# Kernel tuning notes

Measured on AMD Instinct MI355X. Metric: run time of the kernel, lower is better.

The kernel has to match this reference:

```python
import jax, jax.numpy as jnp
import numpy as np

NODE, HIDDEN, BATCH, OUT, BUF = 200, 10, 50, 64, 500
DT = 0.0001
# ParamsJR('JR') defaults (all variances 0 -> constants, not Parameters)
A_, a_, B_, b_ = 3.25, 100.0, 22.0, 50.0
g_, c1_, c2_, c3_, c4_ = 1000.0, 135.0, 135.0 * 0.8, 135.0 * 0.25, 135.0 * 0.25
std_in_, vmax, v0, r_, y0, cy0 = 100.0, 5.0, 6.0, 0.56, 2.0, 5.0
LB, U_UB, NOISE_LB, SAT = 0.01, 500.0, 150.0, 1000.0


def setup_inputs() -> dict:
    key = jax.random.key(0)
    ks = jax.random.split(key, 8)
    inp = jax.random.normal(ks[0], (NODE, HIDDEN, BATCH), dtype=jnp.float32)
    noise_in = jax.random.normal(ks[1], (NODE, HIDDEN, BATCH), dtype=jnp.float32)
    hx = jax.random.uniform(ks[2], (NODE, 6), dtype=jnp.float32)
    hE = jax.random.uniform(ks[3], (NODE, BUF), dtype=jnp.float32)
    sc = jax.random.uniform(ks[4], (NODE, NODE), dtype=jnp.float32)
    w_bb = jax.random.uniform(ks[5], (NODE, NODE), dtype=jnp.float32)  # fitted gains (init 0.05 in torch)
    lm = jax.random.normal(ks[6], (OUT, NODE), dtype=jnp.float32)  # lead-field
    delays = jax.random.randint(ks[7], (NODE, NODE), 0, BUF)  # (dist/(1.5+relu(mu))).int64
    return {"inp": inp, "noise_in": noise_in, "hx": hx, "hE": hE,
            "sc": sc, "w_bb": w_bb, "lm": lm, "delays": delays}


def _sigmoid(x):
    return vmax / (1.0 + jnp.exp(r_ * (v0 - x)))


def _sys2nd(A, a, u, x, v):
    return A * a * u - 2.0 * a * v - a * a * x


def _forward(inp, noise_in, hx, hE, sc, w_bb, lm, delays):
    relu = jax.nn.relu
    A_e, a_e = relu(A_), 1.0 + relu(a_)          # 0*con+relu(A), 1*con+relu(a)
    B_e, b_e = relu(B_), 1.0 + relu(b_)
    g_e, c1e, c2e, c3e, c4e = (LB + relu(g_), LB + relu(c1_), LB + relu(c2_),
                               LB + relu(c3_), LB + relu(c4_))
    std_e = NOISE_LB + relu(std_in_)

    # normalized laplacian-style connectivity
    w = jnp.exp(w_bb) * sc
    wl = jnp.log1p(0.5 * (w + w.T))
    w_n = wl / jnp.linalg.norm(wl)
    dg = -jnp.diag(jnp.sum(w_n, axis=1))          # (node, node)
    rows = jnp.arange(NODE)[:, None]

    def step(carry, xs):
        M, E, I, Mv, Ev, Iv, hEb = carry
        u, noise = xs                              # (node,1) each
        Ed = hEb[rows, delays]                     # Ed[i,j] = hE[i, delays[i,j]]
        LEd = jnp.sum(w_n * Ed.T, axis=1, keepdims=True)  # (node,1)
        rM = _sigmoid(E - I)
        rE = (std_e * noise + g_e * (LEd + dg @ E)
              + c2e * _sigmoid(c1e * M))
        rI = c4e * _sigmoid(c3e * M)
        ddM = M + DT * Mv
        ddE = E + DT * Ev
        ddI = I + DT * Iv
        ddMv = Mv + DT * _sys2nd(A_e, a_e, u + U_UB * jnp.tanh(rM / U_UB), M, Mv)
        ddEv = Ev + DT * _sys2nd(A_e, a_e, U_UB * jnp.tanh(rE / U_UB), E, Ev)
        ddIv = Iv + DT * _sys2nd(B_e, b_e, U_UB * jnp.tanh(rI / U_UB), I, Iv)
        sat = lambda x: SAT * jnp.tanh(x / SAT)
        M, E, I, Mv, Ev, Iv = (sat(ddM), sat(ddE), sat(ddI),
                               sat(ddMv), sat(ddEv), sat(ddIv))
        hEb = jnp.concatenate([M, hEb[:, :-1]], axis=1)  # push pyramidal state into delay buffer
        return (M, E, I, Mv, Ev, Iv, hEb), None

    def tr_step(carry, xs):
        u_tr, n_tr = xs                            # (hidden, node, 1)
        carry, _ = jax.lax.scan(step, carry, (u_tr, n_tr))
        M, E, I, Mv, Ev, Iv, _ = carry
        return carry, (M[:, 0], E[:, 0], I[:, 0], Mv[:, 0], Ev[:, 0], Iv[:, 0])

    M, E, I = hx[:, 0:1], hx[:, 1:2], hx[:, 2:3]
    Mv, Ev, Iv = hx[:, 3:4], hx[:, 4:5], hx[:, 5:6]
    u_all = jnp.transpose(inp, (2, 1, 0))[..., None]       # (batch, hidden, node, 1)
    n_all = jnp.transpose(noise_in, (2, 1, 0))[..., None]
    carry, recs = jax.lax.scan(tr_step, (M, E, I, Mv, Ev, Iv, hE), (u_all, n_all))
    Mb, Eb, Ib, Mvb, Evb, Ivb = recs                       # (batch, node) each

    # lead-field: row-normalize then remove channel mean
    lm_n = lm / jnp.sqrt(jnp.sum(lm ** 2, axis=1, keepdims=True))
    lm_t = lm_n - jnp.mean(lm_n, axis=0, keepdims=True)
    eeg = cy0 * jnp.einsum('on,bn->ob', lm_t, Eb - Ib) - y0  # (output, batch)

    M, E, I, Mv, Ev, Iv, hEb = carry
    current_state = jnp.concatenate([M, E, I, Mv, Ev, Iv], axis=1)
    return eeg, current_state, Eb.T, Ib.T, Mb.T, Evb.T, Ivb.T, Mvb.T, hEb


def reference(inp, noise_in, hx, hE, sc, w_bb, lm, delays):
    return _forward(inp, noise_in, hx, hE, sc, w_bb, lm, delays)
```

## Files before the change

kernel.cpp:

```cpp
#include <hip/hip_runtime.h>
#include <math.h>

#define N_NODE 200
#define RING   512
#define ROWF   545
#define NSTEP  500
#define TB     32
#define NB     16
#define NWG    8
#define NTHR   256
#define JSL    25
#define NEARCAP 32
#define MDEP   36

#define FPBUF   (NWG * N_NODE * TB)
#define OFF_FP  0
#define OFF_BAR (2 * FPBUF)
#define WS_NEED ((size_t)(2 * FPBUF + 64) * 4)

#define SM_RED   0
#define SM_MREC  64
#define SM_US    28864
#define SM_NS    54464
#define SM_LED   80864
#define SM_RING  106464
#define SM_TOTAL 160964
#define SM_LMT   64
#define SM_DIFF  51264

__device__ __forceinline__ float ftanh(float x) {
    float ax = fabsf(x);
    float t  = __expf(-2.0f * ax);
    float r  = __fdividef(1.0f - t, 1.0f + t);
    return copysignf(r, x);
}
__device__ __forceinline__ float sigm(float x) {
    return __fdividef(5.0f, 1.0f + __expf(0.56f * (6.0f - x)));
}
__device__ __forceinline__ float satf(float x) {
    return 1000.0f * ftanh(x * 0.001f);
}

__device__ __forceinline__ void grid_barrier(int* slot, int nwg) {
    __syncthreads();
    if (threadIdx.x == 0) {
        __threadfence();
        __hip_atomic_fetch_add(slot, 1, __ATOMIC_ACQ_REL, __HIP_MEMORY_SCOPE_AGENT);
        while (__hip_atomic_load(slot, __ATOMIC_ACQUIRE, __HIP_MEMORY_SCOPE_AGENT) < nwg) {
            __builtin_amdgcn_s_sleep(2);
        }
        __threadfence();
    }
    __syncthreads();
}

__global__ void zero_bar(int* bar) {
    if (threadIdx.x < 64) bar[threadIdx.x] = 0;
}

__global__ __launch_bounds__(NTHR, 1)
void jansen_fast(const float* __restrict__ inp, const float* __restrict__ noise_in,
                 const float* __restrict__ hx,  const float* __restrict__ hE,
                 const float* __restrict__ sc,  const float* __restrict__ wbb,
                 const float* __restrict__ lm,  const int*   __restrict__ delays,
                 float* __restrict__ out, float* __restrict__ ws)
{
    __shared__ char smem[SM_TOTAL];
    double*   red  = (double*)(smem + SM_RED);
    float*    Mrec = (float*)(smem + SM_MREC);
    unsigned* nOFF = (unsigned*)(smem + SM_US);
    float*    nW   = (float*)(smem + SM_NS);
    float*    uS   = (float*)(smem + SM_US);
    float*    nS   = (float*)(smem + SM_NS);
    float*    LEdS = (float*)(smem + SM_LED);
    float*    ringS= (float*)(smem + SM_RING);

    const int tid = threadIdx.x;
    const int wg  = blockIdx.x;
    const int i   = tid;
    const int jlo = wg * JSL;

    float* fp  = ws + OFF_FP;
    int*   bar = (int*)(ws + OFF_BAR);

    double ssq = 0.0;
    for (int q = tid; q < N_NODE * N_NODE; q += NTHR) {
        int j = q / N_NODE, ii = q - j * N_NODE;
        float w1 = expf(wbb[ii * N_NODE + j]) * sc[ii * N_NODE + j];
        float w2 = expf(wbb[j * N_NODE + ii]) * sc[j * N_NODE + ii];
        float wl = log1pf(0.5f * (w1 + w2));
        ssq += (double)wl * (double)wl;
    }
    #pragma unroll
    for (int off = 32; off > 0; off >>= 1) ssq += __shfl_down(ssq, off, 64);
    if ((tid & 63) == 0) red[tid >> 6] = ssq;

    for (int p = tid; p < JSL * ROWF; p += NTHR) {
        int jl = p / ROWF, x = p - jl * ROWF;
        float v = 0.0f;
        if (x < 544) {
            int dd = (x < RING) ? (511 - x) : (1023 - x);
            if (dd < 500) v = hE[(jlo + jl) * 500 + dd];
        }
        ringS[p] = v;
    }
    for (int p = tid; p < MDEP * N_NODE; p += NTHR) {
        int s = p / N_NODE, j = p - s * N_NODE;
        Mrec[p] = (s >= 4) ? hE[j * 500 + (35 - s)] : 0.0f;
    }
    for (int p = tid; p < NEARCAP * N_NODE; p += NTHR) {
        nOFF[p] = 0u;
        nW[p]   = 0.0f;
    }
    __syncthreads();
    if (tid == 0) {
        double s = 0.0;
        #pragma unroll
        for (int r = 0; r < 8; ++r) s += red[r];
        red[0] = 1.0 / sqrt(s);
    }
    __syncthreads();
    const float inv = (float)red[0];

    float rowsum = 0.0f;
    float M = 0, E = 0, I = 0, Mvv = 0, Evv = 0, Ivv = 0;
    float wreg[JSL];
    int   ereg[JSL];
    #pragma unroll
    for (int jl = 0; jl < JSL; ++jl) { wreg[jl] = 0.0f; ereg[jl] = 0; }
    if (i < N_NODE) {
        int cnt = 0;
        for (int j = 0; j < N_NODE; ++j) {
            float w1 = expf(wbb[i * N_NODE + j]) * sc[i * N_NODE + j];
            float w2 = expf(wbb[j * N_NODE + i]) * sc[j * N_NODE + i];
            float w  = log1pf(0.5f * (w1 + w2)) * inv;
            int d = delays[j * N_NODE + i];
            rowsum += w;
            if (d < NEARCAP && cnt < NEARCAP) {
                nOFF[cnt * N_NODE + i] = (unsigned)((35 - d) * N_NODE + j);
                nW  [cnt * N_NODE + i] = w;
                ++cnt;
            }
        }
        #pragma unroll
        for (int jl = 0; jl < JSL; ++jl) {
            int j = jlo + jl;
            float w1 = expf(wbb[i * N_NODE + j]) * sc[i * N_NODE + j];
            float w2 = expf(wbb[j * N_NODE + i]) * sc[j * N_NODE + i];
            float w  = log1pf(0.5f * (w1 + w2)) * inv;
            int d = delays[j * N_NODE + i];
            wreg[jl] = (d < NEARCAP) ? 0.0f : w;
            ereg[jl] = 511 - d;
        }
        M   = hx[i * 6 + 0]; E   = hx[i * 6 + 1]; I   = hx[i * 6 + 2];
        Mvv = hx[i * 6 + 3]; Evv = hx[i * 6 + 4]; Ivv = hx[i * 6 + 5];
    }

    int   noffR[NEARCAP];
    float nwR[NEARCAP];
    {
        const int ii = (i < N_NODE) ? i : 0;
        #pragma unroll
        for (int n = 0; n < NEARCAP; ++n) {
            noffR[n] = (int)nOFF[n * N_NODE + ii];
            nwR[n]   = nW[n * N_NODE + ii];
        }
    }
    __syncthreads();

    for (int b = 0; b < NB; ++b) {
        const int t0 = b * TB;
        float* fpb = fp + (b & 1) * FPBUF;

        if (i < N_NODE) {
            float ac[TB];
            #pragma unroll
            for (int k = 0; k < TB; ++k) ac[k] = 0.0f;
            #pragma unroll
            for (int jl = 0; jl < JSL; ++jl) {
                float w  = wreg[jl];
                int   p0 = (t0 + ereg[jl]) & 511;
                const float* rb = ringS + jl * ROWF + p0;
                #pragma unroll
                for (int k = 0; k < TB; ++k)
                    ac[k] = fmaf(w, rb[k], ac[k]);
            }
            float4* fpw = (float4*)(fpb + wg * (N_NODE * TB) + i * TB);
            #pragma unroll
            for (int q = 0; q < 8; ++q)
                fpw[q] = make_float4(ac[4*q+0], ac[4*q+1], ac[4*q+2], ac[4*q+3]);

            #pragma unroll
            for (int k = 0; k < TB; ++k) {
                int t = t0 + k;
                float uv = 0.0f, nv = 0.0f;
                if (t < NSTEP) {
                    int bb = t / 10, h = t - 10 * bb;
                    uv = inp     [i * 500 + h * 50 + bb];
                    nv = noise_in[i * 500 + h * 50 + bb];
                }
                uS[k * N_NODE + i] = uv;
                nS[k * N_NODE + i] = nv;
            }
        }

        grid_barrier(bar + b, NWG);

        if (i < N_NODE) {
            const float* basep = fpb + i * TB;
            #pragma unroll
            for (int c = 0; c < 8; ++c) {
                float sx = 0, sy = 0, sz = 0, sw = 0;
                #pragma unroll
                for (int g = 0; g < NWG; ++g) {
                    float4 q = *(const float4*)(basep + g * (N_NODE * TB) + c * 4);
                    sx += q.x; sy += q.y; sz += q.z; sw += q.w;
                }
                LEdS[(c * 4 + 0) * N_NODE + i] = sx;
                LEdS[(c * 4 + 1) * N_NODE + i] = sy;
                LEdS[(c * 4 + 2) * N_NODE + i] = sz;
                LEdS[(c * 4 + 3) * N_NODE + i] = sw;
            }
        }
        __syncthreads();

        const int kmax = (NSTEP - t0 < TB) ? (NSTEP - t0) : TB;
        int s36 = t0 % MDEP;
        int bcur = t0 / 10, hcur = t0 - 10 * bcur;
        const bool ringw = (i >= jlo) && (i < jlo + JSL);
        const int  rbase = (i - jlo) * ROWF;
        for (int k = 0; k < kmax; ++k) {
            const int t = t0 + k;
            if (i < N_NODE) {
                const int base36 = s36 * N_NODE;
                float a0 = LEdS[k * N_NODE + i];
                float a1 = 0.0f, a2 = 0.0f, a3 = 0.0f;
                #pragma unroll
                for (int n = 0; n < NEARCAP; n += 4) {
                    int d0 = base36 + noffR[n+0]; if (d0 >= MDEP*N_NODE) d0 -= MDEP*N_NODE;
                    int d1 = base36 + noffR[n+1]; if (d1 >= MDEP*N_NODE) d1 -= MDEP*N_NODE;
                    int d2 = base36 + noffR[n+2]; if (d2 >= MDEP*N_NODE) d2 -= MDEP*N_NODE;
                    int d3 = base36 + noffR[n+3]; if (d3 >= MDEP*N_NODE) d3 -= MDEP*N_NODE;
                    a0 = fmaf(nwR[n+0], Mrec[d0], a0);
                    a1 = fmaf(nwR[n+1], Mrec[d1], a1);
                    a2 = fmaf(nwR[n+2], Mrec[d2], a2);
                    a3 = fmaf(nwR[n+3], Mrec[d3], a3);
                }
                float LEd = (a0 + a1) + (a2 + a3);
                float u  = uS[k * N_NODE + i];
                float nz = nS[k * N_NODE + i];
                float rM = sigm(E - I);
                float rE = 250.0f * nz + 1000.01f * (LEd - rowsum * E) + 108.01f * sigm(135.01f * M);
                float rI = 33.76f * sigm(33.76f * M);
                float ddM = M + 1e-4f * Mvv;
                float ddE = E + 1e-4f * Evv;
                float ddI = I + 1e-4f * Ivv;
                float uu  = u + 500.0f * ftanh(rM * 0.002f);
                float ddMv = Mvv + 1e-4f * (328.25f * uu - 202.0f * Mvv - 10201.0f * M);
                float uE  = 500.0f * ftanh(rE * 0.002f);
                float ddEv = Evv + 1e-4f * (328.25f * uE - 202.0f * Evv - 10201.0f * E);
                float uI  = 500.0f * ftanh(rI * 0.002f);
                float ddIv = Ivv + 1e-4f * (1122.0f * uI - 102.0f * Ivv - 2601.0f * I);
                M   = satf(ddM);  E   = satf(ddE);  I   = satf(ddI);
                Mvv = satf(ddMv); Evv = satf(ddEv); Ivv = satf(ddIv);
                Mrec[base36 + i] = M;
                if (ringw) {
                    int pt = t & 511;
                    ringS[rbase + pt] = M;
                    if (pt < 32) ringS[rbase + pt + 512] = M;
                }
                if (wg == 0 && hcur == 9) {
                    out[ 4400 + i * 50 + bcur] = E;
                    out[14400 + i * 50 + bcur] = I;
                    out[24400 + i * 50 + bcur] = M;
                    out[34400 + i * 50 + bcur] = Evv;
                    out[44400 + i * 50 + bcur] = Ivv;
                    out[54400 + i * 50 + bcur] = Mvv;
                }
                ++hcur; if (hcur == 10) { hcur = 0; ++bcur; }
                ++s36; if (s36 == MDEP) s36 = 0;
            }
            __syncthreads();
        }
    }

    for (int p = tid; p < JSL * 500; p += NTHR) {
        int jl = p / 500, dd = p - jl * 500;
        out[64400 + (jlo + jl) * 500 + dd] = ringS[jl * ROWF + ((499 - dd) & 511)];
    }
    if (wg != 0) return;

    if (i < N_NODE) {
        out[3200 + i * 6 + 0] = M;
        out[3200 + i * 6 + 1] = E;
        out[3200 + i * 6 + 2] = I;
        out[3200 + i * 6 + 3] = Mvv;
        out[3200 + i * 6 + 4] = Evv;
        out[3200 + i * 6 + 5] = Ivv;
    }

    float* lmt  = (float*)(smem + SM_LMT);
    float* diff = (float*)(smem + SM_DIFF);
    __syncthreads();
    if (tid < 64) {
        float s = 0.0f;
        for (int n = 0; n < N_NODE; ++n) { float v = lm[tid * N_NODE + n]; s += v * v; }
        float ivn = 1.0f / sqrtf(s);
        for (int n = 0; n < N_NODE; ++n) lmt[tid * N_NODE + n] = lm[tid * N_NODE + n] * ivn;
    }
    __syncthreads();
    if (tid < N_NODE) {
        float s = 0.0f;
        for (int o = 0; o < 64; ++o) s += lmt[o * N_NODE + tid];
        s *= (1.0f / 64.0f);
        for (int o = 0; o < 64; ++o) lmt[o * N_NODE + tid] -= s;
    }
    __syncthreads();
    for (int p = tid; p < 10000; p += NTHR) diff[p] = out[4400 + p] - out[14400 + p];
    __syncthreads();
    for (int p = tid; p < 3200; p += NTHR) {
        int o = p / 50, bb = p - o * 50;
        float s = 0.0f;
        for (int n = 0; n < N_NODE; ++n)
            s = fmaf(lmt[o * N_NODE + n], diff[n * 50 + bb], s);
        out[p] = 5.0f * s - 2.0f;
    }
}

__global__ __launch_bounds__(1024, 1)
void jansen_main(const float* __restrict__ inp, const float* __restrict__ noise_in,
                 const float* __restrict__ hx,  const float* __restrict__ hE,
                 const float* __restrict__ sc,  const float* __restrict__ wbb,
                 const float* __restrict__ lm,  const int*   __restrict__ delays,
                 float* __restrict__ out, float* __restrict__ ws)
{
    const int tid = threadIdx.x;
    const int i   = tid & 255;
    const int c   = tid >> 8;

    float* ring = ws;
    float* lmt  = ws + N_NODE * RING;

    __shared__ double red[18];
    __shared__ float  part[4][N_NODE];
    __shared__ float  wn[N_NODE * N_NODE];

    double ssq = 0.0;
    for (int p = tid; p < N_NODE * N_NODE; p += 1024) {
        int r0 = p / N_NODE;
        int cc = p - r0 * N_NODE;
        float w1 = expf(wbb[p]) * sc[p];
        float w2 = expf(wbb[cc * N_NODE + r0]) * sc[cc * N_NODE + r0];
        float v  = log1pf(0.5f * (w1 + w2));
        wn[p] = v;
        ssq += (double)v * (double)v;
    }
    #pragma unroll
    for (int off = 32; off > 0; off >>= 1) ssq += __shfl_down(ssq, off, 64);
    if ((tid & 63) == 0) red[tid >> 6] = ssq;
    __syncthreads();
    if (tid == 0) {
        double s = 0.0;
        for (int k = 0; k < 16; ++k) s += red[k];
        red[16] = 1.0 / sqrt(s);
    }
    __syncthreads();
    const float inv_norm = (float)red[16];
    for (int p = tid; p < N_NODE * N_NODE; p += 1024) wn[p] *= inv_norm;

    for (int p = tid; p < N_NODE * 500; p += 1024) {
        int j = p / 500, dd = p - j * 500;
        ring[j * RING + (511 - dd)] = hE[p];
    }
    if (tid < 64) {
        float s = 0.0f;
        for (int n = 0; n < N_NODE; ++n) { float v = lm[tid * N_NODE + n]; s += v * v; }
        float inv = 1.0f / sqrtf(s);
        for (int n = 0; n < N_NODE; ++n) lmt[tid * N_NODE + n] = lm[tid * N_NODE + n] * inv;
    }
    __syncthreads();
    if (tid < N_NODE) {
        float s = 0.0f;
        for (int o = 0; o < 64; ++o) s += lmt[o * N_NODE + tid];
        s *= (1.0f / 64.0f);
        for (int o = 0; o < 64; ++o) lmt[o * N_NODE + tid] -= s;
    }

    unsigned int dpk[25];
    if (i < N_NODE) {
        #pragma unroll
        for (int r0 = 0; r0 < 25; ++r0) {
            int d0 = delays[(c * 50 + 2 * r0    ) * N_NODE + i];
            int d1 = delays[(c * 50 + 2 * r0 + 1) * N_NODE + i];
            unsigned e0 = (unsigned)((-1 - d0) & 511);
            unsigned e1 = (unsigned)((-1 - d1) & 511);
            dpk[r0] = e0 | (e1 << 16);
        }
    }

    float M = 0, E = 0, I = 0, Mvv = 0, Evv = 0, Ivv = 0, rowsum = 0;
    if (c == 0 && i < N_NODE) {
        M   = hx[i * 6 + 0]; E   = hx[i * 6 + 1]; I   = hx[i * 6 + 2];
        Mvv = hx[i * 6 + 3]; Evv = hx[i * 6 + 4]; Ivv = hx[i * 6 + 5];
    }
    __syncthreads();
    if (c == 0 && i < N_NODE) {
        float s = 0.0f;
        for (int j = 0; j < N_NODE; ++j) s += wn[j * N_NODE + i];
        rowsum = s;
    }

    for (int t = 0; t < NSTEP; ++t) {
        if (i < N_NODE) {
            float acc = 0.0f;
            const float* ringc = ring + c * 50 * RING;
            const float* wnc   = wn + c * 50 * N_NODE + i;
            #pragma unroll
            for (int r0 = 0; r0 < 50; ++r0) {
                unsigned e = (dpk[r0 >> 1] >> ((r0 & 1) << 4)) & 0xffffu;
                int pos = (int)(((unsigned)t + e) & 511u);
                acc = fmaf(wnc[r0 * N_NODE], ringc[r0 * RING + pos], acc);
            }
            part[c][i] = acc;
        }
        __syncthreads();
        if (c == 0 && i < N_NODE) {
            float LEd = part[0][i] + part[1][i] + part[2][i] + part[3][i];
            int b = t / 10, h = t - b * 10;
            float u  = inp     [i * 500 + h * 50 + b];
            float nz = noise_in[i * 500 + h * 50 + b];
            float rM = 5.0f / (1.0f + expf(0.56f * (6.0f - (E - I))));
            float rE = 250.0f * nz + 1000.01f * (LEd - rowsum * E) + 108.01f * (5.0f / (1.0f + expf(0.56f * (6.0f - 135.01f * M))));
            float rI = 33.76f * (5.0f / (1.0f + expf(0.56f * (6.0f - 33.76f * M))));
            float ddM = M + 1e-4f * Mvv;
            float ddE = E + 1e-4f * Evv;
            float ddI = I + 1e-4f * Ivv;
            float uu  = u + 500.0f * tanhf(rM / 500.0f);
            float ddMv = Mvv + 1e-4f * (328.25f * uu - 202.0f * Mvv - 10201.0f * M);
            float uE  = 500.0f * tanhf(rE / 500.0f);
            float ddEv = Evv + 1e-4f * (328.25f * uE - 202.0f * Evv - 10201.0f * E);
            float uI  = 500.0f * tanhf(rI / 500.0f);
            float ddIv = Ivv + 1e-4f * (1122.0f * uI - 102.0f * Ivv - 2601.0f * I);
            M   = 1000.0f * tanhf(ddM / 1000.0f);
            E   = 1000.0f * tanhf(ddE / 1000.0f);
            I   = 1000.0f * tanhf(ddI / 1000.0f);
            Mvv = 1000.0f * tanhf(ddMv / 1000.0f);
            Evv = 1000.0f * tanhf(ddEv / 1000.0f);
            Ivv = 1000.0f * tanhf(ddIv / 1000.0f);
            ring[i * RING + (t & 511)] = M;
            if (h == 9) {
                out[ 4400 + i * 50 + b] = E;
                out[14400 + i * 50 + b] = I;
                out[24400 + i * 50 + b] = M;
                out[34400 + i * 50 + b] = Evv;
                out[44400 + i * 50 + b] = Ivv;
                out[54400 + i * 50 + b] = Mvv;
            }
        }
        __syncthreads();
    }

    if (c == 0 && i < N_NODE) {
        out[3200 + i * 6 + 0] = M;
        out[3200 + i * 6 + 1] = E;
        out[3200 + i * 6 + 2] = I;
        out[3200 + i * 6 + 3] = Mvv;
        out[3200 + i * 6 + 4] = Evv;
        out[3200 + i * 6 + 5] = Ivv;
    }
    for (int p = tid; p < N_NODE * 500; p += 1024) {
        int ii = p / 500, dd = p - ii * 500;
        out[64400 + p] = ring[ii * RING + (499 - dd)];
    }
    __syncthreads();
    for (int p = tid; p < 64 * 50; p += 1024) {
        int o = p / 50, b = p - o * 50;
        float s = 0.0f;
        for (int n = 0; n < N_NODE; ++n)
            s += lmt[o * N_NODE + n] * (out[4400 + n * 50 + b] - out[14400 + n * 50 + b]);
        out[p] = 5.0f * s - 2.0f;
    }
}

extern "C" void kernel_launch(void* const* d_in, const int* in_sizes, int n_in,
                              void* d_out, int out_size, void* d_ws, size_t ws_size,
                              hipStream_t stream) {
    if (ws_size >= WS_NEED) {
        zero_bar<<<1, 64, 0, stream>>>((int*)((float*)d_ws + OFF_BAR));
        jansen_fast<<<NWG, NTHR, 0, stream>>>(
            (const float*)d_in[0], (const float*)d_in[1], (const float*)d_in[2],
            (const float*)d_in[3], (const float*)d_in[4], (const float*)d_in[5],
            (const float*)d_in[6], (const int*)d_in[7],
            (float*)d_out, (float*)d_ws);
    } else {
        jansen_main<<<1, 1024, 0, stream>>>(
            (const float*)d_in[0], (const float*)d_in[1], (const float*)d_in[2],
            (const float*)d_in[3], (const float*)d_in[4], (const float*)d_in[5],
            (const float*)d_in[6], (const int*)d_in[7],
            (float*)d_out, (float*)d_ws);
    }
}
```

Baseline: 1.210 ms.

## Split zero-delay neighbors and precompute next-step near-delay gather one step ahead

```diff
diff --git a/kernel.cpp b/kernel.cpp
--- a/kernel.cpp
+++ b/kernel.cpp
@@ -12,6 +12,7 @@
 #define JSL    25
 #define NEARCAP 32
 #define MDEP   36
+#define MSZ    (MDEP * N_NODE)
 
 #define FPBUF   (NWG * N_NODE * TB)
 #define OFF_FP  0
@@ -59,17 +60,19 @@
 }
 
 __global__ __launch_bounds__(NTHR, 1)
-void jansen_fast(const float* __restrict__ inp, const float* __restrict__ noise_in,
-                 const float* __restrict__ hx,  const float* __restrict__ hE,
-                 const float* __restrict__ sc,  const float* __restrict__ wbb,
-                 const float* __restrict__ lm,  const int*   __restrict__ delays,
-                 float* __restrict__ out, float* __restrict__ ws)
+void jansen_pg(const float* __restrict__ inp, const float* __restrict__ noise_in,
+               const float* __restrict__ hx,  const float* __restrict__ hE,
+               const float* __restrict__ sc,  const float* __restrict__ wbb,
+               const float* __restrict__ lm,  const int*   __restrict__ delays,
+               float* __restrict__ out, float* __restrict__ ws)
 {
     __shared__ char smem[SM_TOTAL];
     double*   red  = (double*)(smem + SM_RED);
     float*    Mrec = (float*)(smem + SM_MREC);
-    unsigned* nOFF = (unsigned*)(smem + SM_US);
-    float*    nW   = (float*)(smem + SM_NS);
+    unsigned* n1OFF = (unsigned*)(smem + SM_US);
+    float*    n1W   = (float*)(smem + SM_NS);
+    unsigned* n0J   = (unsigned*)(smem + SM_LED);
+    float*    n0W   = (float*)(smem + SM_LED + 8 * N_NODE * 4);
     float*    uS   = (float*)(smem + SM_US);
     float*    nS   = (float*)(smem + SM_NS);
     float*    LEdS = (float*)(smem + SM_LED);
@@ -108,9 +111,13 @@
         int s = p / N_NODE, j = p - s * N_NODE;
         Mrec[p] = (s >= 4) ? hE[j * 500 + (35 - s)] : 0.0f;
     }
-    for (int p = tid; p < NEARCAP * N_NODE; p += NTHR) {
-        nOFF[p] = 0u;
-        nW[p]   = 0.0f;
+    for (int p = tid; p < 32 * N_NODE; p += NTHR) {
+        n1OFF[p] = 0u;
+        n1W[p]   = 0.0f;
+    }
+    for (int p = tid; p < 8 * N_NODE; p += NTHR) {
+        n0J[p] = 0u;
+        n0W[p] = 0.0f;
     }
     __syncthreads();
     if (tid == 0) {
@@ -128,18 +135,26 @@
     int   ereg[JSL];
     #pragma unroll
     for (int jl = 0; jl < JSL; ++jl) { wreg[jl] = 0.0f; ereg[jl] = 0; }
+    int cnt0 = 0, cnt1 = 0;
     if (i < N_NODE) {
-        int cnt = 0;
         for (int j = 0; j < N_NODE; ++j) {
             float w1 = expf(wbb[i * N_NODE + j]) * sc[i * N_NODE + j];
             float w2 = expf(wbb[j * N_NODE + i]) * sc[j * N_NODE + i];
             float w  = log1pf(0.5f * (w1 + w2)) * inv;
             int d = delays[j * N_NODE + i];
             rowsum += w;
-            if (d < NEARCAP && cnt < NEARCAP) {
-                nOFF[cnt * N_NODE + i] = (unsigned)((35 - d) * N_NODE + j);
-                nW  [cnt * N_NODE + i] = w;
-                ++cnt;
+            if (d == 0) {
+                if (cnt0 < 8) {
+                    n0J[cnt0 * N_NODE + i] = (unsigned)j;
+                    n0W[cnt0 * N_NODE + i] = w;
+                    ++cnt0;
+                }
+            } else if (d < NEARCAP) {
+                if (cnt1 < 32) {
+                    n1OFF[cnt1 * N_NODE + i] = (unsigned)((35 - d) * N_NODE + j);
+                    n1W  [cnt1 * N_NODE + i] = w;
+                    ++cnt1;
+                }
             }
         }
         #pragma unroll
@@ -156,18 +171,44 @@
         Mvv = hx[i * 6 + 3]; Evv = hx[i * 6 + 4]; Ivv = hx[i * 6 + 5];
     }
 
-    int   noffR[NEARCAP];
-    float nwR[NEARCAP];
+    int   n1off[32]; float n1w[32];
+    int   n0j[8];    float n0w[8];
     {
         const int ii = (i < N_NODE) ? i : 0;
         #pragma unroll
-        for (int n = 0; n < NEARCAP; ++n) {
-            noffR[n] = (int)nOFF[n * N_NODE + ii];
-            nwR[n]   = nW[n * N_NODE + ii];
-        }
-    }
-    __syncthreads();
-
+        for (int n = 0; n < 32; ++n) {
+            n1off[n] = (int)n1OFF[n * N_NODE + ii];
+            n1w[n]   = n1W[n * N_NODE + ii];
+        }
+        #pragma unroll
+        for (int z = 0; z < 8; ++z) {
+            n0j[z] = (int)n0J[z * N_NODE + ii];
+            n0w[z] = n0W[z * N_NODE + ii];
+        }
+    }
+
+    float LEdN = 0.0f;
+    if (i < N_NODE) {
+        float gA = 0.0f, gB = 0.0f, gC = 0.0f, gD = 0.0f;
+        #pragma unroll
+        for (int n = 0; n < 8; ++n) gA = fmaf(n1w[n], Mrec[n1off[n]], gA);
+        if (cnt1 > 8) {
+            #pragma unroll
+            for (int n = 8; n < 16; ++n) gB = fmaf(n1w[n], Mrec[n1off[n]], gB);
+        }
+        if (cnt1 > 16) {
+            #pragma unroll
+            for (int n = 16; n < 24; ++n) gC = fmaf(n1w[n], Mrec[n1off[n]], gC);
+        }
+        if (cnt1 > 24) {
+            #pragma unroll
+            for (int n = 24; n < 32; ++n) gD = fmaf(n1w[n], Mrec[n1off[n]], gD);
+        }
+        LEdN = (gA + gB) + (gC + gD);
+    }
+    __syncthreads();
+
+    int base36 = 0;
     for (int b = 0; b < NB; ++b) {
         const int t0 = b * TB;
         float* fpb = fp + (b & 1) * FPBUF;
@@ -225,30 +266,52 @@
         __syncthreads();
 
         const int kmax = (NSTEP - t0 < TB) ? (NSTEP - t0) : TB;
-        int s36 = t0 % MDEP;
         int bcur = t0 / 10, hcur = t0 - 10 * bcur;
         const bool ringw = (i >= jlo) && (i < jlo + JSL);
         const int  rbase = (i - jlo) * ROWF;
         for (int k = 0; k < kmax; ++k) {
             const int t = t0 + k;
             if (i < N_NODE) {
-                const int base36 = s36 * N_NODE;
-                float a0 = LEdS[k * N_NODE + i];
-                float a1 = 0.0f, a2 = 0.0f, a3 = 0.0f;
-                #pragma unroll
-                for (int n = 0; n < NEARCAP; n += 4) {
-                    int d0 = base36 + noffR[n+0]; if (d0 >= MDEP*N_NODE) d0 -= MDEP*N_NODE;
-                    int d1 = base36 + noffR[n+1]; if (d1 >= MDEP*N_NODE) d1 -= MDEP*N_NODE;
-                    int d2 = base36 + noffR[n+2]; if (d2 >= MDEP*N_NODE) d2 -= MDEP*N_NODE;
-                    int d3 = base36 + noffR[n+3]; if (d3 >= MDEP*N_NODE) d3 -= MDEP*N_NODE;
-                    a0 = fmaf(nwR[n+0], Mrec[d0], a0);
-                    a1 = fmaf(nwR[n+1], Mrec[d1], a1);
-                    a2 = fmaf(nwR[n+2], Mrec[d2], a2);
-                    a3 = fmaf(nwR[n+3], Mrec[d3], a3);
-                }
-                float LEd = (a0 + a1) + (a2 + a3);
+                const int base_prev = (base36 == 0) ? (MSZ - N_NODE) : (base36 - N_NODE);
+                float LEd = LEdN + LEdS[k * N_NODE + i];
                 float u  = uS[k * N_NODE + i];
                 float nz = nS[k * N_NODE + i];
+                #pragma unroll
+                for (int z = 0; z < 4; ++z)
+                    LEd = fmaf(n0w[z], Mrec[base_prev + n0j[z]], LEd);
+                if (cnt0 > 4) {
+                    #pragma unroll
+                    for (int z = 4; z < 8; ++z)
+                        LEd = fmaf(n0w[z], Mrec[base_prev + n0j[z]], LEd);
+                }
+                int base36n = base36 + N_NODE; if (base36n == MSZ) base36n = 0;
+                float gA = 0.0f, gB = 0.0f, gC = 0.0f, gD = 0.0f;
+                #pragma unroll
+                for (int n = 0; n < 8; ++n) {
+                    int a = base36n + n1off[n]; if (a >= MSZ) a -= MSZ;
+                    gA = fmaf(n1w[n], Mrec[a], gA);
+                }
+                if (cnt1 > 8) {
+                    #pragma unroll
+                    for (int n = 8; n < 16; ++n) {
+                        int a = base36n + n1off[n]; if (a >= MSZ) a -= MSZ;
+                        gB = fmaf(n1w[n], Mrec[a], gB);
+                    }
+                }
+                if (cnt1 > 16) {
+                    #pragma unroll
+                    for (int n = 16; n < 24; ++n) {
+                        int a = base36n + n1off[n]; if (a >= MSZ) a -= MSZ;
+                        gC = fmaf(n1w[n], Mrec[a], gC);
+                    }
+                }
+                if (cnt1 > 24) {
+                    #pragma unroll
+                    for (int n = 24; n < 32; ++n) {
+                        int a = base36n + n1off[n]; if (a >= MSZ) a -= MSZ;
+                        gD = fmaf(n1w[n], Mrec[a], gD);
+                    }
+                }
                 float rM = sigm(E - I);
                 float rE = 250.0f * nz + 1000.01f * (LEd - rowsum * E) + 108.01f * sigm(135.01f * M);
                 float rI = 33.76f * sigm(33.76f * M);
@@ -263,6 +326,7 @@
                 float ddIv = Ivv + 1e-4f * (1122.0f * uI - 102.0f * Ivv - 2601.0f * I);
                 M   = satf(ddM);  E   = satf(ddE);  I   = satf(ddI);
                 Mvv = satf(ddMv); Evv = satf(ddEv); Ivv = satf(ddIv);
+                LEdN = (gA + gB) + (gC + gD);
                 Mrec[base36 + i] = M;
                 if (ringw) {
                     int pt = t & 511;
@@ -278,7 +342,7 @@
                     out[54400 + i * 50 + bcur] = Mvv;
                 }
                 ++hcur; if (hcur == 10) { hcur = 0; ++bcur; }
-                ++s36; if (s36 == MDEP) s36 = 0;
+                base36 = base36n;
             }
             __syncthreads();
         }
@@ -487,7 +551,7 @@
                               hipStream_t stream) {
     if (ws_size >= WS_NEED) {
         zero_bar<<<1, 64, 0, stream>>>((int*)((float*)d_ws + OFF_BAR));
-        jansen_fast<<<NWG, NTHR, 0, stream>>>(
+        jansen_pg<<<NWG, NTHR, 0, stream>>>(
             (const float*)d_in[0], (const float*)d_in[1], (const float*)d_in[2],
             (const float*)d_in[3], (const float*)d_in[4], (const float*)d_in[5],
             (const float*)d_in[6], (const int*)d_in[7],
```

After: 1.253 ms. 3.5% more time.

## Split near-delay taps and batch mid-range delayed sums four steps at once

Applied to the files above, without the earlier changes.

```diff
diff --git a/kernel.cpp b/kernel.cpp
--- a/kernel.cpp
+++ b/kernel.cpp
@@ -3,15 +3,17 @@
 
 #define N_NODE 200
 #define RING   512
-#define ROWF   545
+#define ROWF   543
 #define NSTEP  500
 #define TB     32
 #define NB     16
 #define NWG    8
 #define NTHR   256
 #define JSL    25
-#define NEARCAP 32
 #define MDEP   36
+#define MROW   39
+#define HICAP  28
+#define LOCAP  8
 
 #define FPBUF   (NWG * N_NODE * TB)
 #define OFF_FP  0
@@ -20,11 +22,14 @@
 
 #define SM_RED   0
 #define SM_MREC  64
-#define SM_US    28864
-#define SM_NS    54464
-#define SM_LED   80864
-#define SM_RING  106464
-#define SM_TOTAL 160964
+#define SM_UN    31264
+#define SM_LEDS  82464
+#define SM_RING  108064
+#define SM_TOTAL 162364
+#define SM_HIX   SM_UN
+#define SM_HIW   (SM_UN + 22400)
+#define SM_LOX   SM_LEDS
+#define SM_LOW   (SM_LEDS + 6400)
 #define SM_LMT   64
 #define SM_DIFF  51264
 
@@ -59,20 +64,21 @@
 }
 
 __global__ __launch_bounds__(NTHR, 1)
-void jansen_fast(const float* __restrict__ inp, const float* __restrict__ noise_in,
-                 const float* __restrict__ hx,  const float* __restrict__ hE,
-                 const float* __restrict__ sc,  const float* __restrict__ wbb,
-                 const float* __restrict__ lm,  const int*   __restrict__ delays,
-                 float* __restrict__ out, float* __restrict__ ws)
+void jansen_b4(const float* __restrict__ inp, const float* __restrict__ noise_in,
+               const float* __restrict__ hx,  const float* __restrict__ hE,
+               const float* __restrict__ sc,  const float* __restrict__ wbb,
+               const float* __restrict__ lm,  const int*   __restrict__ delays,
+               float* __restrict__ out, float* __restrict__ ws)
 {
     __shared__ char smem[SM_TOTAL];
     double*   red  = (double*)(smem + SM_RED);
     float*    Mrec = (float*)(smem + SM_MREC);
-    unsigned* nOFF = (unsigned*)(smem + SM_US);
-    float*    nW   = (float*)(smem + SM_NS);
-    float*    uS   = (float*)(smem + SM_US);
-    float*    nS   = (float*)(smem + SM_NS);
-    float*    LEdS = (float*)(smem + SM_LED);
+    unsigned* hiX  = (unsigned*)(smem + SM_HIX);
+    float*    hiW  = (float*)(smem + SM_HIW);
+    unsigned* loX  = (unsigned*)(smem + SM_LOX);
+    float*    loW  = (float*)(smem + SM_LOW);
+    float2*   unS  = (float2*)(smem + SM_UN);
+    float*    LEdS = (float*)(smem + SM_LEDS);
     float*    ringS= (float*)(smem + SM_RING);
 
     const int tid = threadIdx.x;
@@ -97,21 +103,15 @@
 
     for (int p = tid; p < JSL * ROWF; p += NTHR) {
         int jl = p / ROWF, x = p - jl * ROWF;
-        float v = 0.0f;
-        if (x < 544) {
-            int dd = (x < RING) ? (511 - x) : (1023 - x);
-            if (dd < 500) v = hE[(jlo + jl) * 500 + dd];
-        }
-        ringS[p] = v;
-    }
-    for (int p = tid; p < MDEP * N_NODE; p += NTHR) {
-        int s = p / N_NODE, j = p - s * N_NODE;
-        Mrec[p] = (s >= 4) ? hE[j * 500 + (35 - s)] : 0.0f;
-    }
-    for (int p = tid; p < NEARCAP * N_NODE; p += NTHR) {
-        nOFF[p] = 0u;
-        nW[p]   = 0.0f;
-    }
+        int dd = (x < RING) ? (511 - x) : (1023 - x);
+        ringS[p] = (dd < 500) ? hE[(jlo + jl) * 500 + dd] : 0.0f;
+    }
+    for (int p = tid; p < N_NODE * MROW; p += NTHR) {
+        int j = p / MROW, s = p - j * MROW;
+        Mrec[p] = (s >= 4 && s < MDEP) ? hE[j * 500 + (35 - s)] : 0.0f;
+    }
+    for (int p = tid; p < HICAP * N_NODE; p += NTHR) { hiX[p] = 0u; hiW[p] = 0.0f; }
+    for (int p = tid; p < LOCAP * N_NODE; p += NTHR) { loX[p] = 0u; loW[p] = 0.0f; }
     __syncthreads();
     if (tid == 0) {
         double s = 0.0;
@@ -128,18 +128,26 @@
     int   ereg[JSL];
     #pragma unroll
     for (int jl = 0; jl < JSL; ++jl) { wreg[jl] = 0.0f; ereg[jl] = 0; }
+    int cntLo = 0, cntHi = 0;
     if (i < N_NODE) {
-        int cnt = 0;
         for (int j = 0; j < N_NODE; ++j) {
             float w1 = expf(wbb[i * N_NODE + j]) * sc[i * N_NODE + j];
             float w2 = expf(wbb[j * N_NODE + i]) * sc[j * N_NODE + i];
             float w  = log1pf(0.5f * (w1 + w2)) * inv;
             int d = delays[j * N_NODE + i];
             rowsum += w;
-            if (d < NEARCAP && cnt < NEARCAP) {
-                nOFF[cnt * N_NODE + i] = (unsigned)((35 - d) * N_NODE + j);
-                nW  [cnt * N_NODE + i] = w;
-                ++cnt;
+            if (d < 4) {
+                if (cntLo < LOCAP) {
+                    loX[cntLo * N_NODE + i] = (unsigned)((j * MROW) << 6) | (unsigned)(35 - d);
+                    loW[cntLo * N_NODE + i] = w;
+                    ++cntLo;
+                }
+            } else if (d < 32) {
+                if (cntHi < HICAP) {
+                    hiX[cntHi * N_NODE + i] = (unsigned)((j * MROW) << 6) | (unsigned)(35 - d);
+                    hiW[cntHi * N_NODE + i] = w;
+                    ++cntHi;
+                }
             }
         }
         #pragma unroll
@@ -149,24 +157,31 @@
             float w2 = expf(wbb[j * N_NODE + i]) * sc[j * N_NODE + i];
             float w  = log1pf(0.5f * (w1 + w2)) * inv;
             int d = delays[j * N_NODE + i];
-            wreg[jl] = (d < NEARCAP) ? 0.0f : w;
+            wreg[jl] = (d < 32) ? 0.0f : w;
             ereg[jl] = 511 - d;
         }
         M   = hx[i * 6 + 0]; E   = hx[i * 6 + 1]; I   = hx[i * 6 + 2];
         Mvv = hx[i * 6 + 3]; Evv = hx[i * 6 + 4]; Ivv = hx[i * 6 + 5];
     }
 
-    int   noffR[NEARCAP];
-    float nwR[NEARCAP];
+    int hix[HICAP]; float hiw[HICAP];
+    int lox[LOCAP]; float low[LOCAP];
     {
         const int ii = (i < N_NODE) ? i : 0;
         #pragma unroll
-        for (int n = 0; n < NEARCAP; ++n) {
-            noffR[n] = (int)nOFF[n * N_NODE + ii];
-            nwR[n]   = nW[n * N_NODE + ii];
-        }
-    }
-    __syncthreads();
+        for (int n = 0; n < HICAP; ++n) {
+            hix[n] = (int)hiX[n * N_NODE + ii];
+            hiw[n] = hiW[n * N_NODE + ii];
+        }
+        #pragma unroll
+        for (int z = 0; z < LOCAP; ++z) {
+            lox[z] = (int)loX[z * N_NODE + ii];
+            low[z] = loW[z * N_NODE + ii];
+        }
+    }
+    __syncthreads();
+
+    const int rowM = (i < N_NODE ? i : 0) * MROW;
 
     for (int b = 0; b < NB; ++b) {
         const int t0 = b * TB;
@@ -199,28 +214,28 @@
                     uv = inp     [i * 500 + h * 50 + bb];
                     nv = noise_in[i * 500 + h * 50 + bb];
                 }
-                uS[k * N_NODE + i] = uv;
-                nS[k * N_NODE + i] = nv;
+                unS[k * N_NODE + i] = make_float2(uv, nv);
             }
         }
 
         grid_barrier(bar + b, NWG);
 
         if (i < N_NODE) {
-            const float* basep = fpb + i * TB;
-            #pragma unroll
-            for (int c = 0; c < 8; ++c) {
-                float sx = 0, sy = 0, sz = 0, sw = 0;
+            float sA[TB];
+            #pragma unroll
+            for (int k = 0; k < TB; ++k) sA[k] = 0.0f;
+            #pragma unroll
+            for (int g = 0; g < NWG; ++g) {
+                const float4* row = (const float4*)(fpb + g * (N_NODE * TB) + i * TB);
                 #pragma unroll
-                for (int g = 0; g < NWG; ++g) {
-                    float4 q = *(const float4*)(basep + g * (N_NODE * TB) + c * 4);
-                    sx += q.x; sy += q.y; sz += q.z; sw += q.w;
-                }
-                LEdS[(c * 4 + 0) * N_NODE + i] = sx;
-                LEdS[(c * 4 + 1) * N_NODE + i] = sy;
-                LEdS[(c * 4 + 2) * N_NODE + i] = sz;
-                LEdS[(c * 4 + 3) * N_NODE + i] = sw;
-            }
+                for (int c = 0; c < 8; ++c) {
+                    float4 qv = row[c];
+                    sA[4*c+0] += qv.x; sA[4*c+1] += qv.y;
+                    sA[4*c+2] += qv.z; sA[4*c+3] += qv.w;
+                }
+            }
+            #pragma unroll
+            for (int k = 0; k < TB; ++k) LEdS[k * N_NODE + i] = sA[k];
         }
         __syncthreads();
 
@@ -229,58 +244,104 @@
         int bcur = t0 / 10, hcur = t0 - 10 * bcur;
         const bool ringw = (i >= jlo) && (i < jlo + JSL);
         const int  rbase = (i - jlo) * ROWF;
-        for (int k = 0; k < kmax; ++k) {
-            const int t = t0 + k;
+        for (int k4 = 0; k4 < kmax; k4 += 4) {
+            float g0 = 0, g1 = 0, g2 = 0, g3 = 0;
             if (i < N_NODE) {
-                const int base36 = s36 * N_NODE;
-                float a0 = LEdS[k * N_NODE + i];
-                float a1 = 0.0f, a2 = 0.0f, a3 = 0.0f;
                 #pragma unroll
-                for (int n = 0; n < NEARCAP; n += 4) {
-                    int d0 = base36 + noffR[n+0]; if (d0 >= MDEP*N_NODE) d0 -= MDEP*N_NODE;
-                    int d1 = base36 + noffR[n+1]; if (d1 >= MDEP*N_NODE) d1 -= MDEP*N_NODE;
-                    int d2 = base36 + noffR[n+2]; if (d2 >= MDEP*N_NODE) d2 -= MDEP*N_NODE;
-                    int d3 = base36 + noffR[n+3]; if (d3 >= MDEP*N_NODE) d3 -= MDEP*N_NODE;
-                    a0 = fmaf(nwR[n+0], Mrec[d0], a0);
-                    a1 = fmaf(nwR[n+1], Mrec[d1], a1);
-                    a2 = fmaf(nwR[n+2], Mrec[d2], a2);
-                    a3 = fmaf(nwR[n+3], Mrec[d3], a3);
-                }
-                float LEd = (a0 + a1) + (a2 + a3);
-                float u  = uS[k * N_NODE + i];
-                float nz = nS[k * N_NODE + i];
-                float rM = sigm(E - I);
-                float rE = 250.0f * nz + 1000.01f * (LEd - rowsum * E) + 108.01f * sigm(135.01f * M);
-                float rI = 33.76f * sigm(33.76f * M);
-                float ddM = M + 1e-4f * Mvv;
-                float ddE = E + 1e-4f * Evv;
-                float ddI = I + 1e-4f * Ivv;
-                float uu  = u + 500.0f * ftanh(rM * 0.002f);
-                float ddMv = Mvv + 1e-4f * (328.25f * uu - 202.0f * Mvv - 10201.0f * M);
-                float uE  = 500.0f * ftanh(rE * 0.002f);
-                float ddEv = Evv + 1e-4f * (328.25f * uE - 202.0f * Evv - 10201.0f * E);
-                float uI  = 500.0f * ftanh(rI * 0.002f);
-                float ddIv = Ivv + 1e-4f * (1122.0f * uI - 102.0f * Ivv - 2601.0f * I);
-                M   = satf(ddM);  E   = satf(ddE);  I   = satf(ddI);
-                Mvv = satf(ddMv); Evv = satf(ddEv); Ivv = satf(ddIv);
-                Mrec[base36 + i] = M;
-                if (ringw) {
-                    int pt = t & 511;
-                    ringS[rbase + pt] = M;
-                    if (pt < 32) ringS[rbase + pt + 512] = M;
-                }
-                if (wg == 0 && hcur == 9) {
-                    out[ 4400 + i * 50 + bcur] = E;
-                    out[14400 + i * 50 + bcur] = I;
-                    out[24400 + i * 50 + bcur] = M;
-                    out[34400 + i * 50 + bcur] = Evv;
-                    out[44400 + i * 50 + bcur] = Ivv;
-                    out[54400 + i * 50 + bcur] = Mvv;
-                }
-                ++hcur; if (hcur == 10) { hcur = 0; ++bcur; }
-                ++s36; if (s36 == MDEP) s36 = 0;
-            }
-            __syncthreads();
+                for (int n = 0; n < 8; ++n) {
+                    int tmp = (hix[n] & 63) + s36; if (tmp >= MDEP) tmp -= MDEP;
+                    const float* rp = Mrec + (hix[n] >> 6) + tmp;
+                    float w = hiw[n];
+                    g0 = fmaf(w, rp[0], g0); g1 = fmaf(w, rp[1], g1);
+                    g2 = fmaf(w, rp[2], g2); g3 = fmaf(w, rp[3], g3);
+                }
+                if (cntHi > 8) {
+                    #pragma unroll
+                    for (int n = 8; n < 16; ++n) {
+                        int tmp = (hix[n] & 63) + s36; if (tmp >= MDEP) tmp -= MDEP;
+                        const float* rp = Mrec + (hix[n] >> 6) + tmp;
+                        float w = hiw[n];
+                        g0 = fmaf(w, rp[0], g0); g1 = fmaf(w, rp[1], g1);
+                        g2 = fmaf(w, rp[2], g2); g3 = fmaf(w, rp[3], g3);
+                    }
+                }
+                if (cntHi > 16) {
+                    #pragma unroll
+                    for (int n = 16; n < 24; ++n) {
+                        int tmp = (hix[n] & 63) + s36; if (tmp >= MDEP) tmp -= MDEP;
+                        const float* rp = Mrec + (hix[n] >> 6) + tmp;
+                        float w = hiw[n];
+                        g0 = fmaf(w, rp[0], g0); g1 = fmaf(w, rp[1], g1);
+                        g2 = fmaf(w, rp[2], g2); g3 = fmaf(w, rp[3], g3);
+                    }
+                }
+                if (cntHi > 24) {
+                    #pragma unroll
+                    for (int n = 24; n < 28; ++n) {
+                        int tmp = (hix[n] & 63) + s36; if (tmp >= MDEP) tmp -= MDEP;
+                        const float* rp = Mrec + (hix[n] >> 6) + tmp;
+                        float w = hiw[n];
+                        g0 = fmaf(w, rp[0], g0); g1 = fmaf(w, rp[1], g1);
+                        g2 = fmaf(w, rp[2], g2); g3 = fmaf(w, rp[3], g3);
+                    }
+                }
+            }
+            #pragma unroll
+            for (int q = 0; q < 4; ++q) {
+                const int k = k4 + q;
+                if (i < N_NODE) {
+                    int scur = s36 + q; if (scur >= MDEP) scur -= MDEP;
+                    float LEd = (q == 0) ? g0 : (q == 1) ? g1 : (q == 2) ? g2 : g3;
+                    LEd += LEdS[k * N_NODE + i];
+                    #pragma unroll
+                    for (int z = 0; z < 4; ++z) {
+                        int tmp = (lox[z] & 63) + scur; if (tmp >= MDEP) tmp -= MDEP;
+                        LEd = fmaf(low[z], Mrec[(lox[z] >> 6) + tmp], LEd);
+                    }
+                    if (cntLo > 4) {
+                        #pragma unroll
+                        for (int z = 4; z < 8; ++z) {
+                            int tmp = (lox[z] & 63) + scur; if (tmp >= MDEP) tmp -= MDEP;
+                            LEd = fmaf(low[z], Mrec[(lox[z] >> 6) + tmp], LEd);
+                        }
+                    }
+                    float2 un = unS[k * N_NODE + i];
+                    float u  = un.x;
+                    float nz = un.y;
+                    float rM = sigm(E - I);
+                    float rE = 250.0f * nz + 1000.01f * (LEd - rowsum * E) + 108.01f * sigm(135.01f * M);
+                    float rI = 33.76f * sigm(33.76f * M);
+                    float ddM = M + 1e-4f * Mvv;
+                    float ddE = E + 1e-4f * Evv;
+                    float ddI = I + 1e-4f * Ivv;
+                    float uu  = u + 500.0f * ftanh(rM * 0.002f);
+                    float ddMv = Mvv + 1e-4f * (328.25f * uu - 202.0f * Mvv - 10201.0f * M);
+                    float uE  = 500.0f * ftanh(rE * 0.002f);
+                    float ddEv = Evv + 1e-4f * (328.25f * uE - 202.0f * Evv - 10201.0f * E);
+                    float uI  = 500.0f * ftanh(rI * 0.002f);
+                    float ddIv = Ivv + 1e-4f * (1122.0f * uI - 102.0f * Ivv - 2601.0f * I);
+                    M   = satf(ddM);  E   = satf(ddE);  I   = satf(ddI);
+                    Mvv = satf(ddMv); Evv = satf(ddEv); Ivv = satf(ddIv);
+                    Mrec[rowM + scur] = M;
+                    if (scur < 3) Mrec[rowM + scur + MDEP] = M;
+                    if (ringw) {
+                        int pt = (t0 + k) & 511;
+                        ringS[rbase + pt] = M;
+                        if (pt < 31) ringS[rbase + pt + 512] = M;
+                    }
+                    if (wg == 0 && hcur == 9) {
+                        out[ 4400 + i * 50 + bcur] = E;
+                        out[14400 + i * 50 + bcur] = I;
+                        out[24400 + i * 50 + bcur] = M;
+                        out[34400 + i * 50 + bcur] = Evv;
+                        out[44400 + i * 50 + bcur] = Ivv;
+                        out[54400 + i * 50 + bcur] = Mvv;
+                    }
+                    ++hcur; if (hcur == 10) { hcur = 0; ++bcur; }
+                }
+                __syncthreads();
+            }
+            s36 += 4; if (s36 >= MDEP) s36 -= MDEP;
         }
     }
 
@@ -487,7 +548,7 @@
                               hipStream_t stream) {
     if (ws_size >= WS_NEED) {
         zero_bar<<<1, 64, 0, stream>>>((int*)((float*)d_ws + OFF_BAR));
-        jansen_fast<<<NWG, NTHR, 0, stream>>>(
+        jansen_b4<<<NWG, NTHR, 0, stream>>>(
             (const float*)d_in[0], (const float*)d_in[1], (const float*)d_in[2],
             (const float*)d_in[3], (const float*)d_in[4], (const float*)d_in[5],
             (const float*)d_in[6], (const int*)d_in[7],
```

Measured after the change: 1.315 ms. 1.09x slower.
